# Performance work log

Measured on AMD Instinct MI355X. Metric: run time of the kernel, lower is better.

Reference implementation:

```python
import jax, jax.numpy as jnp
import numpy as np

EPS = 1e-08
F_DIM = 512


def setup_inputs() -> dict:
    key = jax.random.key(0)
    ks = jax.random.split(key, 7)
    N, F = 50000, F_DIM
    q = jax.random.normal(ks[0], (N, 1, F), dtype=jnp.float32)
    mu = jax.random.normal(ks[1], (N, 3, F), dtype=jnp.float32)
    # Xavier-ish scaled params
    W_mix = jax.random.normal(ks[2], (2 * F, F), dtype=jnp.float32) * (1.0 / np.sqrt(F))
    W1 = jax.random.normal(ks[3], (F, 2 * F), dtype=jnp.float32) * (1.0 / np.sqrt(2 * F))
    b1 = jnp.zeros((F,), dtype=jnp.float32)
    W2 = jax.random.normal(ks[4], (3 * F, F), dtype=jnp.float32) * (1.0 / np.sqrt(F))
    b2 = jnp.zeros((3 * F,), dtype=jnp.float32)
    return {"q": q, "mu": mu, "W_mix": W_mix, "W1": W1, "b1": b1, "W2": W2, "b2": b2}


def reference(q, mu, W_mix, W1, b1, W2, b2):
    F = q.shape[-1]
    # mu_channel_mix: [N,3,F] @ [F,2F] -> [N,3,2F]
    mu_mix = jnp.einsum('ndf,gf->ndg', mu, W_mix)
    mu_V, mu_W = mu_mix[..., :F], mu_mix[..., F:]
    # vector norm over Cartesian axis -> [N,1,F]
    mu_Vn = jnp.sqrt(jnp.sum(mu_V * mu_V, axis=-2, keepdims=True) + EPS)
    ctx = jnp.concatenate([q, mu_Vn], axis=-1)  # [N,1,2F]
    h = jax.nn.silu(jnp.einsum('nsf,gf->nsg', ctx, W1) + b1)  # [N,1,F]
    x = jnp.einsum('nsf,gf->nsg', h, W2) + b2  # [N,1,3F]
    dq_intra = x[..., :F]
    dmu_intra = x[..., F:2 * F] * mu_W  # broadcast [N,1,F]*[N,3,F]
    dqmu_intra = x[..., 2 * F:] * jnp.sum(mu_V * mu_W, axis=1, keepdims=True)
    q_out = q + dq_intra + dqmu_intra
    mu_out = mu + dmu_intra
    return (q_out, mu_out)
```

## Files before the change

kernel.cpp:

```cpp
#include <hip/hip_runtime.h>
#include <stdint.h>

#define NN 50000
#define QWORDS 25600000

typedef __attribute__((ext_vector_type(8))) short bf16x8;
typedef __attribute__((ext_vector_type(4))) float f32x4;

__device__ __forceinline__ uint32_t f2bf(float x){
  uint32_t u = __builtin_bit_cast(uint32_t, x);
  u += 0x7FFFu + ((u >> 16) & 1u);
  return u >> 16;
}
__device__ __forceinline__ float bf2f(uint32_t b){
  uint32_t u = b << 16;
  return __builtin_bit_cast(float, u);
}
__device__ __forceinline__ void gload16(const uint16_t* g, uint16_t* l){
  __builtin_amdgcn_global_load_lds(
      (const __attribute__((address_space(1))) uint32_t*)g,
      (__attribute__((address_space(3))) uint32_t*)l, 16, 0, 0);
}
__device__ __forceinline__ f32x4 mfma16(bf16x8 a, bf16x8 b, f32x4 c){
  return __builtin_amdgcn_mfma_f32_16x16x32_bf16(a, b, c, 0, 0, 0);
}

#define FENCE() asm volatile("" ::: "memory")

__global__ void k_convert(const float* __restrict__ wmix, const float* __restrict__ w1,
                          const float* __restrict__ w2, uint16_t* __restrict__ dst){
  int i = blockIdx.x * 256 + threadIdx.x;
  int e = i << 2;
  const float* s; int o;
  if (e < 524288)       { s = wmix; o = e; }
  else if (e < 1048576) { s = w1;   o = e - 524288; }
  else                  { s = w2;   o = e - 1048576; }
  f32x4 v = *(const f32x4*)(s + o);
  uint2 pk;
  pk.x = f2bf(v[0]) | (f2bf(v[1]) << 16);
  pk.y = f2bf(v[2]) | (f2bf(v[3]) << 16);
  *(uint2*)(dst + e) = pk;
}

__global__ __launch_bounds__(256, 2)
void k_gemm1(const float* __restrict__ mu, const uint16_t* __restrict__ wmixb,
             uint16_t* __restrict__ qh, float* __restrict__ muW){
  __shared__ uint16_t As[2][12288];
  __shared__ uint16_t Bs[2][8192];
  const int tid  = threadIdx.x;
  const int lane = tid & 63;
  const int w    = tid >> 6;
  const int orig = blockIdx.x;
  const int j    = (orig & 7) * 782 + (orig >> 3);
  const int f0   = (j & 7) * 64;
  const int n0   = (j >> 3) * 64;
  const int si = tid >> 4;
  const int sc = (tid & 15) * 4;

  f32x4 ar[12];
  auto A_LOAD = [&](int ks){
    const int k0 = ks * 64;
    #pragma unroll
    for (int blk=0; blk<4; ++blk)
      #pragma unroll
      for (int d=0; d<3; ++d){
        int n = n0 + blk*16 + si;
        int g = (n < NN ? n : NN-1)*3 + d;
        ar[blk*3+d] = *(const f32x4*)(mu + (size_t)g*512 + k0 + sc);
      }
  };
  auto A_WRITE = [&](int buf){
    #pragma unroll
    for (int blk=0; blk<4; ++blk)
      #pragma unroll
      for (int d=0; d<3; ++d){
        int r = blk*48 + d*16 + si;
        f32x4 v = ar[blk*3+d];
        uint2 pk;
        pk.x = f2bf(v[0]) | (f2bf(v[1]) << 16);
        pk.y = f2bf(v[2]) | (f2bf(v[3]) << 16);
        *(uint2*)&As[buf][r*64 + (sc ^ ((r&7)<<3))] = pk;
      }
  };
  auto B_ISSUE = [&](int ks, int buf){
    const int k0 = ks * 64;
    #pragma unroll
    for (int jj=0; jj<4; ++jj){
      int jb = w*4 + jj;
      int row = jb*8 + (lane>>3);
      int g = (row < 64) ? (f0 + row) : (448 + f0 + row);
      int srcc = ((lane&7) ^ ((lane>>3)&7)) * 8;
      gload16(wmixb + (size_t)g*512 + k0 + srcc, &Bs[buf][jb*512]);
    }
  };

  const f32x4 z4 = {0.f,0.f,0.f,0.f};
  f32x4 acc[3][8];
  #pragma unroll
  for (int d=0; d<3; ++d)
    #pragma unroll
    for (int nt=0; nt<8; ++nt) acc[d][nt] = z4;

  A_LOAD(0); B_ISSUE(0, 0); A_WRITE(0);
  for (int ks=0; ks<8; ++ks){
    const int cur = ks & 1;
    __syncthreads();
    if (ks < 7){ A_LOAD(ks+1); B_ISSUE(ks+1, cur^1); }
    #pragma unroll
    for (int kf=0; kf<2; ++kf){
      int kc = kf*32 + (lane>>4)*8;
      bf16x8 af[3];
      #pragma unroll
      for (int d=0; d<3; ++d){
        int r = w*48 + d*16 + (lane&15);
        af[d] = *(const bf16x8*)&As[cur][r*64 + (kc ^ ((r&7)<<3))];
      }
      #pragma unroll
      for (int nt=0; nt<8; ++nt){
        int rr = nt*16 + (lane&15);
        bf16x8 bf = *(const bf16x8*)&Bs[cur][rr*64 + (kc ^ ((rr&7)<<3))];
        #pragma unroll
        for (int d=0; d<3; ++d)
          acc[d][nt] = mfma16(af[d], bf, acc[d][nt]);
      }
    }
    if (ks < 7) A_WRITE(cur^1);
  }

  const int rb4 = (lane >> 4) * 4;
  #pragma unroll
  for (int c=0; c<4; ++c){
    #pragma unroll
    for (int jx=0; jx<4; ++jx){
      int n = n0 + w*16 + rb4 + jx;
      if (n >= NN) continue;
      int f = f0 + c*16 + (lane & 15);
      float v0 = acc[0][c][jx],   v1 = acc[1][c][jx],   v2 = acc[2][c][jx];
      float u0 = acc[0][c+4][jx], u1 = acc[1][c+4][jx], u2 = acc[2][c+4][jx];
      float vn = sqrtf(v0*v0 + v1*v1 + v2*v2 + 1e-8f);
      float dt = v0*u0 + v1*u1 + v2*u2;
      qh[(size_t)n*1024 + f]       = (uint16_t)f2bf(vn);
      qh[(size_t)n*1024 + 512 + f] = (uint16_t)f2bf(dt);
      size_t mb = (size_t)n*1536 + f;
      muW[mb] = u0; muW[mb+512] = u1; muW[mb+1024] = u2;
    }
  }
}

__global__ __launch_bounds__(256, 2)
void k_gemm2(const float* __restrict__ q, const uint16_t* __restrict__ w1b,
             const float* __restrict__ b1, uint16_t* __restrict__ qh){
  __shared__ uint16_t A2[2][2048];
  __shared__ uint16_t B2[2][16384];
  const int tid  = threadIdx.x;
  const int lane = tid & 63;
  const int w    = tid >> 6;
  const int wm   = w >> 1;
  const int wn   = w & 1;
  const int n0   = blockIdx.x * 64;

  f32x4 qa0, qa1;
  auto QA_LOAD = [&](int s){
    int k0 = s*32;
    int row = tid >> 2, ch = tid & 3;
    int nc = (n0 + row < NN) ? n0 + row : NN-1;
    qa0 = *(const f32x4*)(q + (size_t)nc*512 + k0 + ch*8);
    qa1 = *(const f32x4*)(q + (size_t)nc*512 + k0 + ch*8 + 4);
  };
  auto QA_WRITE = [&](int buf){
    int row = tid >> 2, ch = tid & 3;
    uint4 pk;
    pk.x = f2bf(qa0[0]) | (f2bf(qa0[1]) << 16);
    pk.y = f2bf(qa0[2]) | (f2bf(qa0[3]) << 16);
    pk.z = f2bf(qa1[0]) | (f2bf(qa1[1]) << 16);
    pk.w = f2bf(qa1[2]) | (f2bf(qa1[3]) << 16);
    *(uint4*)&A2[buf][row*32 + ((ch ^ (row&3)))*8] = pk;
  };
  auto VA_ISSUE = [&](int s, int buf){
    int k0v = (s-16)*32;
    int row = w*16 + (lane>>2);
    int nc = (n0 + row < NN) ? n0 + row : NN-1;
    int srcch = (lane&3) ^ (row&3);
    gload16(qh + (size_t)nc*1024 + k0v + srcch*8, &A2[buf][w*512]);
  };
  auto B_ISSUE = [&](int s, int buf){
    int k0 = s*32;
    #pragma unroll
    for (int jj=0; jj<8; ++jj){
      int j = w*8 + jj;
      int row = j*16 + (lane>>2);
      int srcch = (lane&3) ^ (row&3);
      gload16(w1b + (size_t)row*1024 + k0 + srcch*8, &B2[buf][j*512]);
    }
  };

  const f32x4 z4 = {0.f,0.f,0.f,0.f};
  f32x4 acc2[2][16];
  #pragma unroll
  for (int mt=0; mt<2; ++mt)
    #pragma unroll
    for (int nt=0; nt<16; ++nt) acc2[mt][nt] = z4;

  QA_LOAD(0); B_ISSUE(0, 0); QA_WRITE(0);
  for (int s=0; s<32; ++s){
    const int cur = s & 1;
    __syncthreads();
    if (s < 31){
      if (s+1 < 16) QA_LOAD(s+1); else VA_ISSUE(s+1, cur^1);
      B_ISSUE(s+1, cur^1);
    }
    {
      int kc = (lane>>4)*8;
      bf16x8 a[2];
      #pragma unroll
      for (int mt=0; mt<2; ++mt){
        int r = wm*32 + mt*16 + (lane&15);
        a[mt] = *(const bf16x8*)&A2[cur][r*32 + (kc ^ ((r&3)<<3))];
      }
      #pragma unroll
      for (int nt=0; nt<16; ++nt){
        int rr = wn*256 + nt*16 + (lane&15);
        bf16x8 b = *(const bf16x8*)&B2[cur][rr*32 + (kc ^ ((rr&3)<<3))];
        acc2[0][nt] = mfma16(a[0], b, acc2[0][nt]);
        acc2[1][nt] = mfma16(a[1], b, acc2[1][nt]);
      }
    }
    if (s < 31 && s+1 < 16) QA_WRITE(cur^1);
  }

  const int rb4 = (lane >> 4) * 4;
  #pragma unroll
  for (int nt=0; nt<16; ++nt){
    int col = wn*256 + nt*16 + (lane&15);
    float bb = b1[col];
    #pragma unroll
    for (int mt=0; mt<2; ++mt)
      #pragma unroll
      for (int j=0; j<4; ++j){
        int n = n0 + wm*32 + mt*16 + rb4 + j;
        if (n < NN){
          float x = acc2[mt][nt][j] + bb;
          float sv = x / (1.f + __expf(-x));
          qh[(size_t)n*1024 + col] = (uint16_t)f2bf(sv);
        }
      }
  }
}

__global__ __launch_bounds__(512, 4)
void k_gemm3(const float* __restrict__ q, const float* __restrict__ mu,
             const uint16_t* __restrict__ w2b, const float* __restrict__ b2,
             float* __restrict__ dout){
  __shared__ uint16_t Hs[32*512];
  __shared__ uint16_t B3[2][12288];
  const int tid  = threadIdx.x;
  const int lane = tid & 63;
  const int w    = tid >> 6;
  const int wm   = w >> 2;
  const int wn   = w & 3;
  const int n0   = blockIdx.x * 32;
  const uint16_t* qh = (const uint16_t*)dout;
  float* mout = dout + (size_t)QWORDS;
  const int l15 = lane & 15;
  const int rb4 = (lane >> 4) * 4;
  const f32x4 z4 = {0.f,0.f,0.f,0.f};

  #pragma unroll
  for (int i=0; i<4; ++i){
    int row = w*4 + i;
    int nc = (n0 + row < NN) ? n0 + row : NN-1;
    gload16(qh + (size_t)nc*1024 + (size_t)((lane ^ (row&7))*8), &Hs[row*512]);
  }

  auto B_ISSUE = [&](int it, int ks, uint16_t* slot){
    #pragma unroll
    for (int jj=0; jj<3; ++jj){
      int j = w*3 + jj;
      int rr = j*8 + (lane>>3);
      int s3 = rr >> 6, fi = rr & 63;
      int g = s3*512 + it*64 + fi;
      gload16(w2b + (size_t)g*512 + ks*64 + ((lane&7) ^ (rr&7))*8, slot + j*512);
    }
  };
  B_ISSUE(0, 0, B3[0]);

  float dtv[4], qv[4], muv[3][4], mwv[3][4];
  float bb0=0.f, bb1=0.f, bb2=0.f;
  int   fq = 0;
  f32x4 acc3[3];

#define K3_MFMA(KS) do{ \
    const uint16_t* bsl = B3[(KS)&1]; \
    __builtin_amdgcn_s_setprio(1); \
    _Pragma("unroll") \
    for (int kf=0; kf<2; ++kf){ \
      int r = wm*16 + l15; \
      int ch = ((KS)*8 + kf*4 + (lane>>4)) ^ (r&7); \
      bf16x8 a = *(const bf16x8*)&Hs[r*512 + ch*8]; \
      _Pragma("unroll") \
      for (int s3=0; s3<3; ++s3){ \
        int rr = s3*64 + wn*16 + l15; \
        int chb = (kf*4 + (lane>>4)) ^ (rr&7); \
        bf16x8 b = *(const bf16x8*)&bsl[rr*64 + chb*8]; \
        acc3[s3] = mfma16(a, b, acc3[s3]); \
      } \
    } \
    __builtin_amdgcn_s_setprio(0); \
  } while(0)

  #pragma unroll 1
  for (int it=0; it<8; ++it){
    if (it) { asm volatile("s_waitcnt vmcnt(16)" ::: "memory"); }
    else    { asm volatile("s_waitcnt vmcnt(0)"  ::: "memory"); }
    __builtin_amdgcn_s_barrier();
    B_ISSUE(it, 1, B3[1]);
    FENCE();
    {
      #pragma unroll
      for (int s3=0; s3<3; ++s3) acc3[s3] = z4;
      fq = it*64 + wn*16 + l15;
      bb0 = b2[fq]; bb1 = b2[512+fq]; bb2 = b2[1024+fq];
      #pragma unroll
      for (int p=0; p<4; ++p){
        int n = n0 + wm*16 + rb4 + p;
        int nc = n < NN ? n : NN-1;
        dtv[p] = bf2f(qh[(size_t)nc*1024 + 512 + fq]);
        qv[p]  = q[(size_t)nc*512 + fq];
      }
    }
    FENCE();
    K3_MFMA(0);

    asm volatile("s_waitcnt vmcnt(11)" ::: "memory");
    __builtin_amdgcn_s_barrier();
    B_ISSUE(it, 2, B3[0]);
    FENCE();
    {
      #pragma unroll
      for (int p=0; p<4; ++p){
        int n = n0 + wm*16 + rb4 + p;
        int nc = n < NN ? n : NN-1;
        size_t mb = (size_t)nc*1536 + fq;
        muv[0][p] = mu[mb]; muv[1][p] = mu[mb+512]; muv[2][p] = mu[mb+1024];
      }
    }
    FENCE();
    K3_MFMA(1);

    asm volatile("s_waitcnt vmcnt(12)" ::: "memory");
    __builtin_amdgcn_s_barrier();
    B_ISSUE(it, 3, B3[1]);
    FENCE();
    {
      #pragma unroll
      for (int p=0; p<4; ++p){
        int n = n0 + wm*16 + rb4 + p;
        int nc = n < NN ? n : NN-1;
        size_t mb = (size_t)nc*1536 + fq;
        mwv[0][p] = mout[mb]; mwv[1][p] = mout[mb+512]; mwv[2][p] = mout[mb+1024];
      }
    }
    FENCE();
    K3_MFMA(2);

    asm volatile("s_waitcnt vmcnt(12)" ::: "memory");
    __builtin_amdgcn_s_barrier();
    B_ISSUE(it, 4, B3[0]);
    FENCE();
    K3_MFMA(3);

    asm volatile("s_waitcnt vmcnt(0)" ::: "memory");
    __builtin_amdgcn_s_barrier();
    B_ISSUE(it, 5, B3[1]);
    FENCE();
    K3_MFMA(4);

    asm volatile("s_waitcnt vmcnt(0)" ::: "memory");
    __builtin_amdgcn_s_barrier();
    B_ISSUE(it, 6, B3[0]);
    FENCE();
    K3_MFMA(5);

    asm volatile("s_waitcnt vmcnt(0)" ::: "memory");
    __builtin_amdgcn_s_barrier();
    B_ISSUE(it, 7, B3[1]);
    FENCE();
    K3_MFMA(6);

    asm volatile("s_waitcnt vmcnt(0)" ::: "memory");
    __builtin_amdgcn_s_barrier();
    if (it < 7) B_ISSUE(it+1, 0, B3[0]);
    FENCE();
    K3_MFMA(7);
    {
      #pragma unroll
      for (int p=0; p<4; ++p){
        int n = n0 + wm*16 + rb4 + p;
        if (n < NN){
          float x0 = acc3[0][p] + bb0;
          float x1 = acc3[1][p] + bb1;
          float x2 = acc3[2][p] + bb2;
          dout[(size_t)n*512 + fq] = qv[p] + x0 + x2*dtv[p];
          size_t mb = (size_t)n*1536 + fq;
          mout[mb]      = muv[0][p] + x1*mwv[0][p];
          mout[mb+512]  = muv[1][p] + x1*mwv[1][p];
          mout[mb+1024] = muv[2][p] + x1*mwv[2][p];
        }
      }
    }
  }
#undef K3_MFMA
}

extern "C" void kernel_launch(void* const* d_in, const int* in_sizes, int n_in,
                              void* d_out, int out_size, void* d_ws, size_t ws_size,
                              hipStream_t stream){
  (void)in_sizes; (void)n_in; (void)out_size; (void)ws_size;
  const float* q    = (const float*)d_in[0];
  const float* mu   = (const float*)d_in[1];
  const float* wmix = (const float*)d_in[2];
  const float* w1   = (const float*)d_in[3];
  const float* b1   = (const float*)d_in[4];
  const float* w2   = (const float*)d_in[5];
  const float* b2   = (const float*)d_in[6];
  uint16_t* wb = (uint16_t*)d_ws;
  float* dout = (float*)d_out;

  hipLaunchKernelGGL(k_convert, dim3(1792), dim3(256), 0, stream, wmix, w1, w2, wb);
  hipLaunchKernelGGL(k_gemm1, dim3(6256), dim3(256), 0, stream,
                     mu, wb, (uint16_t*)d_out, dout + (size_t)QWORDS);
  hipLaunchKernelGGL(k_gemm2, dim3(782), dim3(256), 0, stream,
                     q, wb + 524288, b1, (uint16_t*)d_out);
  hipLaunchKernelGGL(k_gemm3, dim3(1563), dim3(512), 0, stream,
                     q, mu, wb + 1048576, b2, dout);
}
```

Before: 929.8 us.

## Split gemm1 tile across 8 waves with 512-thread blocks

After: 895.2 us. -3.7%, faster.

```diff
diff --git a/kernel.cpp b/kernel.cpp
--- a/kernel.cpp
+++ b/kernel.cpp
@@ -42,7 +42,7 @@
   *(uint2*)(dst + e) = pk;
 }
 
-__global__ __launch_bounds__(256, 2)
+__global__ __launch_bounds__(512, 4)
 void k_gemm1(const float* __restrict__ mu, const uint16_t* __restrict__ wmixb,
              uint16_t* __restrict__ qh, float* __restrict__ muW){
   __shared__ uint16_t As[2][12288];
@@ -50,43 +50,43 @@
   const int tid  = threadIdx.x;
   const int lane = tid & 63;
   const int w    = tid >> 6;
+  const int wn   = w & 3;
+  const int wf   = w >> 2;
   const int orig = blockIdx.x;
   const int j    = (orig & 7) * 782 + (orig >> 3);
   const int f0   = (j & 7) * 64;
   const int n0   = (j >> 3) * 64;
-  const int si = tid >> 4;
-  const int sc = (tid & 15) * 4;
-
-  f32x4 ar[12];
+  const int lrow = tid >> 4;
+  const int lcol = (tid & 15) * 4;
+
+  f32x4 ar[6];
   auto A_LOAD = [&](int ks){
     const int k0 = ks * 64;
     #pragma unroll
-    for (int blk=0; blk<4; ++blk)
-      #pragma unroll
-      for (int d=0; d<3; ++d){
-        int n = n0 + blk*16 + si;
-        int g = (n < NN ? n : NN-1)*3 + d;
-        ar[blk*3+d] = *(const f32x4*)(mu + (size_t)g*512 + k0 + sc);
-      }
+    for (int p=0; p<6; ++p){
+      int r = p*32 + lrow;
+      int d = r >> 6, nrow = r & 63;
+      int n = n0 + nrow;
+      int g = (n < NN ? n : NN-1)*3 + d;
+      ar[p] = *(const f32x4*)(mu + (size_t)g*512 + k0 + lcol);
+    }
   };
   auto A_WRITE = [&](int buf){
     #pragma unroll
-    for (int blk=0; blk<4; ++blk)
-      #pragma unroll
-      for (int d=0; d<3; ++d){
-        int r = blk*48 + d*16 + si;
-        f32x4 v = ar[blk*3+d];
-        uint2 pk;
-        pk.x = f2bf(v[0]) | (f2bf(v[1]) << 16);
-        pk.y = f2bf(v[2]) | (f2bf(v[3]) << 16);
-        *(uint2*)&As[buf][r*64 + (sc ^ ((r&7)<<3))] = pk;
-      }
+    for (int p=0; p<6; ++p){
+      int r = p*32 + lrow;
+      f32x4 v = ar[p];
+      uint2 pk;
+      pk.x = f2bf(v[0]) | (f2bf(v[1]) << 16);
+      pk.y = f2bf(v[2]) | (f2bf(v[3]) << 16);
+      *(uint2*)&As[buf][r*64 + (lcol ^ ((r&7)<<3))] = pk;
+    }
   };
   auto B_ISSUE = [&](int ks, int buf){
     const int k0 = ks * 64;
     #pragma unroll
-    for (int jj=0; jj<4; ++jj){
-      int jb = w*4 + jj;
+    for (int jj=0; jj<2; ++jj){
+      int jb = w*2 + jj;
       int row = jb*8 + (lane>>3);
       int g = (row < 64) ? (f0 + row) : (448 + f0 + row);
       int srcc = ((lane&7) ^ ((lane>>3)&7)) * 8;
@@ -95,11 +95,11 @@
   };
 
   const f32x4 z4 = {0.f,0.f,0.f,0.f};
-  f32x4 acc[3][8];
+  f32x4 acc[3][4];
   #pragma unroll
   for (int d=0; d<3; ++d)
     #pragma unroll
-    for (int nt=0; nt<8; ++nt) acc[d][nt] = z4;
+    for (int nt=0; nt<4; ++nt) acc[d][nt] = z4;
 
   A_LOAD(0); B_ISSUE(0, 0); A_WRITE(0);
   for (int ks=0; ks<8; ++ks){
@@ -112,12 +112,13 @@
       bf16x8 af[3];
       #pragma unroll
       for (int d=0; d<3; ++d){
-        int r = w*48 + d*16 + (lane&15);
+        int r = d*64 + wn*16 + (lane&15);
         af[d] = *(const bf16x8*)&As[cur][r*64 + (kc ^ ((r&7)<<3))];
       }
       #pragma unroll
-      for (int nt=0; nt<8; ++nt){
-        int rr = nt*16 + (lane&15);
+      for (int nt=0; nt<4; ++nt){
+        int ntg = wf*2 + (nt&1) + (nt>>1)*4;
+        int rr = ntg*16 + (lane&15);
         bf16x8 bf = *(const bf16x8*)&Bs[cur][rr*64 + (kc ^ ((rr&7)<<3))];
         #pragma unroll
         for (int d=0; d<3; ++d)
@@ -129,14 +130,14 @@
 
   const int rb4 = (lane >> 4) * 4;
   #pragma unroll
-  for (int c=0; c<4; ++c){
+  for (int c=0; c<2; ++c){
     #pragma unroll
     for (int jx=0; jx<4; ++jx){
-      int n = n0 + w*16 + rb4 + jx;
+      int n = n0 + wn*16 + rb4 + jx;
       if (n >= NN) continue;
-      int f = f0 + c*16 + (lane & 15);
+      int f = f0 + (wf*2 + c)*16 + (lane & 15);
       float v0 = acc[0][c][jx],   v1 = acc[1][c][jx],   v2 = acc[2][c][jx];
-      float u0 = acc[0][c+4][jx], u1 = acc[1][c+4][jx], u2 = acc[2][c+4][jx];
+      float u0 = acc[0][c+2][jx], u1 = acc[1][c+2][jx], u2 = acc[2][c+2][jx];
       float vn = sqrtf(v0*v0 + v1*v1 + v2*v2 + 1e-8f);
       float dt = v0*u0 + v1*u1 + v2*u2;
       qh[(size_t)n*1024 + f]       = (uint16_t)f2bf(vn);
@@ -427,7 +428,7 @@
   float* dout = (float*)d_out;
 
   hipLaunchKernelGGL(k_convert, dim3(1792), dim3(256), 0, stream, wmix, w1, w2, wb);
-  hipLaunchKernelGGL(k_gemm1, dim3(6256), dim3(256), 0, stream,
+  hipLaunchKernelGGL(k_gemm1, dim3(6256), dim3(512), 0, stream,
                      mu, wb, (uint16_t*)d_out, dout + (size_t)QWORDS);
   hipLaunchKernelGGL(k_gemm2, dim3(782), dim3(256), 0, stream,
                      q, wb + 524288, b1, (uint16_t*)d_out);
```
